# Optimization experiments

Measured on AMD Instinct MI355X. Metric: run time of the kernel, lower is better.

The kernel has to match this reference:

```python
import jax, jax.numpy as jnp
import numpy as np

TOPK = 8  # args.cache_k


def setup_inputs() -> dict:
    key = jax.random.key(0)
    k1, k2, k3 = jax.random.split(key, 3)
    B, N, L, DK, DV = 32, 20000, 20, 512, 512
    query = jax.random.normal(k1, (B, DK), dtype=jnp.float32)
    keys = jax.random.normal(k2, (N, DK), dtype=jnp.float32)
    values = jax.random.normal(k3, (N, L, DV), dtype=jnp.float32)
    return {"query": query, "keys": keys, "values": values}


def reference(query, keys, values):
    # Dot-product attention of query [B, dk] against cache keys [N, dk]
    dk = keys.shape[-1]
    scores = jnp.einsum('bd,nd->bn', query, keys) / jnp.sqrt(jnp.asarray(dk, query.dtype))
    attn = jax.nn.softmax(scores, axis=-1)          # [B, N]
    topk_w, topk_idx = jax.lax.top_k(attn, TOPK)    # [B, k]
    topk_w = topk_w.reshape(-1)                     # [B*k]
    topk_idx = topk_idx.reshape(-1)                 # [B*k]
    # Vectorized replacement of the per-index python loop + torch.cat:
    outputs = values[topk_idx]                      # [B*k, L, dv]
    return topk_w, outputs
```

## Files before the change

kernel.cpp:

```cpp
#include <hip/hip_runtime.h>
#include <math.h>


#define TOPK 8
#define DKD 512
#define NEG  -1.0e30f

typedef __attribute__((ext_vector_type(8))) short short8;
typedef __attribute__((ext_vector_type(4))) float f32x4;

__device__ inline unsigned short f2bf(float x) {
    unsigned int u = __float_as_uint(x);
    u = (u + 0x7fffu + ((u >> 16) & 1u)) >> 16;
    return (unsigned short)u;
}

__device__ inline void wave_argmax(float& v, int& i) {
    #pragma unroll
    for (int off = 1; off < 64; off <<= 1) {
        float ov = __shfl_xor(v, off);
        int   oi = __shfl_xor(i, off);
        if (ov > v || (ov == v && oi < i)) { v = ov; i = oi; }
    }
}

__device__ inline void top8_insert(float (&v)[8], int (&ji)[8], float x, int gi) {
    if (x > v[7]) {
        bool g[8];
        #pragma unroll
        for (int k = 0; k < 8; ++k) g[k] = (x > v[k]);
        #pragma unroll
        for (int k = 7; k >= 1; --k) {
            v[k]  = g[k] ? (g[k - 1] ? v[k - 1] : x)  : v[k];
            ji[k] = g[k] ? (g[k - 1] ? ji[k - 1] : gi) : ji[k];
        }
        v[0]  = g[0] ? x  : v[0];
        ji[0] = g[0] ? gi : ji[0];
    }
}

__global__ __launch_bounds__(256) void score_part_kernel(
    const float* __restrict__ q, const float* __restrict__ keys,
    float* __restrict__ pmg, float* __restrict__ psg,
    float* __restrict__ cvg, int* __restrict__ cig, int N, int NTB)
{
    const int tid  = threadIdx.x;
    const int lane = tid & 63;
    const int wid  = tid >> 6;
    const float scale = 0.04419417382415922f;

    __shared__ short qs[32][DKD + 8];
    __shared__ float S[32][65];

    #pragma unroll
    for (int i = 0; i < 16; ++i) {
        const int idx = i * 256 + tid;
        const int row = idx >> 7;
        const int c4  = idx & 127;
        float4 v = *reinterpret_cast<const float4*>(&q[row * DKD + c4 * 4]);
        ushort4 h;
        h.x = f2bf(v.x); h.y = f2bf(v.y); h.z = f2bf(v.z); h.w = f2bf(v.w);
        *reinterpret_cast<ushort4*>(&qs[row][c4 * 4]) = h;
    }
    __syncthreads();

    {
        const int col = lane & 15;
        const int kg  = lane >> 4;
        const int n0  = blockIdx.x * 64 + wid * 16;

        f32x4 acc0 = {0.f, 0.f, 0.f, 0.f};
        f32x4 acc1 = {0.f, 0.f, 0.f, 0.f};

        int nrow = n0 + col;
        const bool valid = (nrow < N);
        if (!valid) nrow = N - 1;
        const float* krow = keys + (size_t)nrow * DKD + kg * 8;
        const short* s0 = &qs[col][kg * 8];
        const short* s1 = &qs[col + 16][kg * 8];

        #pragma unroll 4
        for (int ks = 0; ks < 16; ++ks) {
            const int d = ks * 32;
            float4 ka = *reinterpret_cast<const float4*>(krow + d);
            float4 kb = *reinterpret_cast<const float4*>(krow + d + 4);
            short8 fh;
            fh[0] = (short)f2bf(ka.x); fh[1] = (short)f2bf(ka.y);
            fh[2] = (short)f2bf(ka.z); fh[3] = (short)f2bf(ka.w);
            fh[4] = (short)f2bf(kb.x); fh[5] = (short)f2bf(kb.y);
            fh[6] = (short)f2bf(kb.z); fh[7] = (short)f2bf(kb.w);
            short8 a0 = *reinterpret_cast<const short8*>(s0 + d);
            short8 a1 = *reinterpret_cast<const short8*>(s1 + d);
            acc0 = __builtin_amdgcn_mfma_f32_16x16x32_bf16(a0, fh, acc0, 0, 0, 0);
            acc1 = __builtin_amdgcn_mfma_f32_16x16x32_bf16(a1, fh, acc1, 0, 0, 0);
        }

        #pragma unroll
        for (int j = 0; j < 4; ++j) {
            const int r = kg * 4 + j;
            S[r][wid * 16 + col]      = valid ? acc0[j] * scale : NEG;
            S[r + 16][wid * 16 + col] = valid ? acc1[j] * scale : NEG;
        }
    }
    __syncthreads();

    {
        const int r = tid >> 3;
        const int g = tid & 7;
        float m = NEG, s = 0.f;
        float v[8]; int ji[8];
        #pragma unroll
        for (int k = 0; k < 8; ++k) { v[k] = NEG; ji[k] = 0x7ffffffe; }

        #pragma unroll
        for (int e = 0; e < 8; ++e) {
            const int c  = g * 8 + e;
            const float x = S[r][c];
            const int  gi = blockIdx.x * 64 + c;
            if (x > -5e29f) {
                const float nm = fmaxf(m, x);
                s = s * __expf(m - nm) + __expf(x - nm);
                m = nm;
                top8_insert(v, ji, x, gi);
            }
        }

        #pragma unroll
        for (int off = 1; off < 8; off <<= 1) {
            float om = __shfl_xor(m, off), os = __shfl_xor(s, off);
            float M2 = fmaxf(m, om);
            s = s * __expf(m - M2) + os * __expf(om - M2);
            m = M2;
        }

        float sel_v[8]; int sel_i[8];
        #pragma unroll
        for (int rr = 0; rr < 8; ++rr) {
            float mv = v[0]; int mi = ji[0];
            #pragma unroll
            for (int off = 1; off < 8; off <<= 1) {
                float ov = __shfl_xor(mv, off);
                int   oi = __shfl_xor(mi, off);
                if (ov > mv || (ov == mv && oi < mi)) { mv = ov; mi = oi; }
            }
            if (v[0] == mv && ji[0] == mi) {
                #pragma unroll
                for (int k = 0; k < 7; ++k) { v[k] = v[k + 1]; ji[k] = ji[k + 1]; }
                v[7] = NEG; ji[7] = 0x7ffffffe;
            }
            sel_v[rr] = mv; sel_i[rr] = mi;
        }

        if (g == 0) {
            const size_t base = (size_t)r * NTB + blockIdx.x;
            pmg[base] = m; psg[base] = s;
            #pragma unroll
            for (int k = 0; k < 8; ++k) {
                cvg[base * 8 + k] = sel_v[k];
                cig[base * 8 + k] = sel_i[k];
            }
        }
    }
}

__global__ __launch_bounds__(256) void row_merge_kernel(
    const float* __restrict__ pmg, const float* __restrict__ psg,
    const float* __restrict__ cvg, const int* __restrict__ cig,
    const float* __restrict__ q, const float* __restrict__ keys,
    float* __restrict__ out_w, int* __restrict__ tidx, int NTB)
{
    const int b    = blockIdx.x;
    const int tid  = threadIdx.x;
    const int lane = tid & 63;
    const int wid  = tid >> 6;
    const float scale = 0.04419417382415922f;

    __shared__ float lm[4], ls[4], lcv[4][TOPK];
    __shared__ int   lci[4][TOPK];

    float m = NEG, s = 0.f;
    float v[8]; int ji[8];
    #pragma unroll
    for (int k = 0; k < 8; ++k) { v[k] = NEG; ji[k] = 0x7ffffffe; }

    for (int tb = tid; tb < NTB; tb += 256) {
        const size_t base = (size_t)b * NTB + tb;
        const float pm_t = pmg[base], ps_t = psg[base];
        const float M2 = fmaxf(m, pm_t);
        s = s * __expf(m - M2) + ps_t * __expf(pm_t - M2);
        m = M2;
        #pragma unroll
        for (int k = 0; k < 8; ++k) {
            top8_insert(v, ji, cvg[base * 8 + k], cig[base * 8 + k]);
        }
    }

    #pragma unroll
    for (int off = 1; off < 64; off <<= 1) {
        float om = __shfl_xor(m, off), os = __shfl_xor(s, off);
        float M2 = fmaxf(m, om);
        s = s * __expf(m - M2) + os * __expf(om - M2);
        m = M2;
    }

    float selv = 0.f; int seli = 0;
    #pragma unroll
    for (int r = 0; r < TOPK; ++r) {
        float mv = v[0]; int mi = ji[0];
        wave_argmax(mv, mi);
        if (v[0] == mv && ji[0] == mi) {
            #pragma unroll
            for (int k = 0; k < TOPK - 1; ++k) { v[k] = v[k + 1]; ji[k] = ji[k + 1]; }
            v[TOPK - 1] = NEG; ji[TOPK - 1] = 0x7ffffffe;
        }
        if (lane == r) { selv = mv; seli = mi; }
    }

    if (lane == 0) { lm[wid] = m; ls[wid] = s; }
    if (lane < TOPK) { lcv[wid][lane] = selv; lci[wid][lane] = seli; }
    __syncthreads();

    if (wid != 0) return;

    float M = lm[0], S = ls[0];
    #pragma unroll
    for (int cc = 1; cc < 4; ++cc) {
        float M2 = fmaxf(M, lm[cc]);
        S = S * __expf(M - M2) + ls[cc] * __expf(lm[cc] - M2);
        M = M2;
    }

    float vv = (lane < 32) ? lcv[lane >> 3][lane & 7] : NEG;
    int   ii = (lane < 32) ? lci[lane >> 3][lane & 7] : 0x7ffffffe;
    int   si = 0x7ffffffe;
    #pragma unroll
    for (int r = 0; r < 12; ++r) {
        float mv = vv; int mi = ii;
        wave_argmax(mv, mi);
        if (vv == mv && ii == mi) vv = NEG;
        if (lane == r) si = mi;
    }

    float4 qa = *reinterpret_cast<const float4*>(q + (size_t)b * DKD + lane * 8);
    float4 qb = *reinterpret_cast<const float4*>(q + (size_t)b * DKD + lane * 8 + 4);
    float exv = NEG;
    #pragma unroll
    for (int r = 0; r < 12; ++r) {
        const int cand = __shfl(si, r);
        const float* kr = keys + (size_t)cand * DKD + lane * 8;
        float4 k1 = *reinterpret_cast<const float4*>(kr);
        float4 k2 = *reinterpret_cast<const float4*>(kr + 4);
        float p = qa.x * k1.x + qa.y * k1.y + qa.z * k1.z + qa.w * k1.w
                + qb.x * k2.x + qb.y * k2.y + qb.z * k2.z + qb.w * k2.w;
        #pragma unroll
        for (int off = 1; off < 64; off <<= 1) p += __shfl_xor(p, off);
        if (lane == r) exv = p * scale;
    }

    float fv = (lane < 12) ? exv : NEG;
    int   fi = (lane < 12) ? si : 0x7ffffffe;
    #pragma unroll
    for (int r = 0; r < TOPK; ++r) {
        float mv = fv; int mi = fi;
        wave_argmax(mv, mi);
        if (fv == mv && fi == mi) fv = NEG;
        if (lane == r) {
            out_w[b * TOPK + r] = __expf(mv - M) / S;
            tidx[b * TOPK + r]  = mi;
        }
    }
}

__global__ __launch_bounds__(256) void gather_kernel(
    const float* __restrict__ values, const int* __restrict__ idx,
    float* __restrict__ out, int LDV)
{
    const int bk  = blockIdx.x >> 2;
    const int qtr = blockIdx.x & 3;
    const int id = idx[bk];
    const float4* src = reinterpret_cast<const float4*>(values + (size_t)id * LDV);
    float4*       dst = reinterpret_cast<float4*>(out + (size_t)bk * LDV);
    const int n4 = LDV >> 2;
    const int qn = n4 >> 2;
    for (int i = qtr * qn + threadIdx.x; i < (qtr + 1) * qn; i += 256)
        dst[i] = src[i];
}

extern "C" void kernel_launch(void* const* d_in, const int* in_sizes, int n_in,
                              void* d_out, int out_size, void* d_ws, size_t ws_size,
                              hipStream_t stream) {
    const float* q      = (const float*)d_in[0];
    const float* keys   = (const float*)d_in[1];
    const float* values = (const float*)d_in[2];

    const int B   = in_sizes[0] / DKD;
    const int N   = in_sizes[1] / DKD;
    const int LDV = (int)((long long)in_sizes[2] / N);
    const int NTB = (N + 63) / 64;

    float* out   = (float*)d_out;
    float* out_w = out;
    float* out_v = out + (size_t)B * TOPK;

    char* wsb = (char*)d_ws;
    size_t off = 0;
    float* pmg = (float*)(wsb + off); off += (size_t)B * NTB * sizeof(float);
    float* psg = (float*)(wsb + off); off += (size_t)B * NTB * sizeof(float);
    float* cvg = (float*)(wsb + off); off += (size_t)B * NTB * 8 * sizeof(float);
    int*   cig = (int*)(wsb + off);   off += (size_t)B * NTB * 8 * sizeof(int);
    int*   tidx = (int*)(wsb + off);  off += (size_t)B * TOPK * sizeof(int);

    score_part_kernel<<<NTB, 256, 0, stream>>>(q, keys, pmg, psg, cvg, cig, N, NTB);
    row_merge_kernel<<<B, 256, 0, stream>>>(pmg, psg, cvg, cig, q, keys, out_w, tidx, NTB);
    gather_kernel<<<B * TOPK * 4, 256, 0, stream>>>(values, tidx, out_v, LDV);
}
```

Baseline: 48.69 us.

## Fuse row merge into gather kernel by recomputing merge per gather block

Merges the row-merge and gather kernels into one launch: each of the B*TOPK*4 gather blocks redundantly recomputes its row's top-k merge (reading all partials, rescoring 12 candidates), then copies its quarter of the selected value row. This removes one kernel launch and the workspace round-trip for indices, at the cost of 32x redundant merge work per row. It also fully unrolls the score loop and sets min-blocks-per-EU on the score kernel.

```diff
diff --git a/kernel.cpp b/kernel.cpp
--- a/kernel.cpp
+++ b/kernel.cpp
@@ -39,7 +39,7 @@
     }
 }
 
-__global__ __launch_bounds__(256) void score_part_kernel(
+__global__ __launch_bounds__(256, 1) void score_part_kernel(
     const float* __restrict__ q, const float* __restrict__ keys,
     float* __restrict__ pmg, float* __restrict__ psg,
     float* __restrict__ cvg, int* __restrict__ cig, int N, int NTB)
@@ -79,7 +79,7 @@
         const short* s0 = &qs[col][kg * 8];
         const short* s1 = &qs[col + 16][kg * 8];
 
-        #pragma unroll 4
+        #pragma unroll
         for (int ks = 0; ks < 16; ++ks) {
             const int d = ks * 32;
             float4 ka = *reinterpret_cast<const float4*>(krow + d);
@@ -163,13 +163,17 @@
     }
 }
 
-__global__ __launch_bounds__(256) void row_merge_kernel(
+__global__ __launch_bounds__(256) void merge_gather_kernel(
     const float* __restrict__ pmg, const float* __restrict__ psg,
     const float* __restrict__ cvg, const int* __restrict__ cig,
     const float* __restrict__ q, const float* __restrict__ keys,
-    float* __restrict__ out_w, int* __restrict__ tidx, int NTB)
+    const float* __restrict__ values,
+    float* __restrict__ out_w, float* __restrict__ out_v, int NTB, int LDV)
 {
-    const int b    = blockIdx.x;
+    const int bk   = blockIdx.x >> 2;
+    const int qtr  = blockIdx.x & 3;
+    const int b    = bk >> 3;
+    const int krk  = bk & 7;
     const int tid  = threadIdx.x;
     const int lane = tid & 63;
     const int wid  = tid >> 6;
@@ -177,6 +181,7 @@
 
     __shared__ float lm[4], ls[4], lcv[4][TOPK];
     __shared__ int   lci[4][TOPK];
+    __shared__ int   s_id;
 
     float m = NEG, s = 0.f;
     float v[8]; int ji[8];
@@ -220,69 +225,64 @@
     if (lane < TOPK) { lcv[wid][lane] = selv; lci[wid][lane] = seli; }
     __syncthreads();
 
-    if (wid != 0) return;
-
-    float M = lm[0], S = ls[0];
-    #pragma unroll
-    for (int cc = 1; cc < 4; ++cc) {
-        float M2 = fmaxf(M, lm[cc]);
-        S = S * __expf(M - M2) + ls[cc] * __expf(lm[cc] - M2);
-        M = M2;
-    }
-
-    float vv = (lane < 32) ? lcv[lane >> 3][lane & 7] : NEG;
-    int   ii = (lane < 32) ? lci[lane >> 3][lane & 7] : 0x7ffffffe;
-    int   si = 0x7ffffffe;
-    #pragma unroll
-    for (int r = 0; r < 12; ++r) {
-        float mv = vv; int mi = ii;
-        wave_argmax(mv, mi);
-        if (vv == mv && ii == mi) vv = NEG;
-        if (lane == r) si = mi;
-    }
-
-    float4 qa = *reinterpret_cast<const float4*>(q + (size_t)b * DKD + lane * 8);
-    float4 qb = *reinterpret_cast<const float4*>(q + (size_t)b * DKD + lane * 8 + 4);
-    float exv = NEG;
-    #pragma unroll
-    for (int r = 0; r < 12; ++r) {
-        const int cand = __shfl(si, r);
-        const float* kr = keys + (size_t)cand * DKD + lane * 8;
-        float4 k1 = *reinterpret_cast<const float4*>(kr);
-        float4 k2 = *reinterpret_cast<const float4*>(kr + 4);
-        float p = qa.x * k1.x + qa.y * k1.y + qa.z * k1.z + qa.w * k1.w
-                + qb.x * k2.x + qb.y * k2.y + qb.z * k2.z + qb.w * k2.w;
-        #pragma unroll
-        for (int off = 1; off < 64; off <<= 1) p += __shfl_xor(p, off);
-        if (lane == r) exv = p * scale;
-    }
-
-    float fv = (lane < 12) ? exv : NEG;
-    int   fi = (lane < 12) ? si : 0x7ffffffe;
-    #pragma unroll
-    for (int r = 0; r < TOPK; ++r) {
-        float mv = fv; int mi = fi;
-        wave_argmax(mv, mi);
-        if (fv == mv && fi == mi) fv = NEG;
-        if (lane == r) {
-            out_w[b * TOPK + r] = __expf(mv - M) / S;
-            tidx[b * TOPK + r]  = mi;
-        }
-    }
-}
-
-__global__ __launch_bounds__(256) void gather_kernel(
-    const float* __restrict__ values, const int* __restrict__ idx,
-    float* __restrict__ out, int LDV)
-{
-    const int bk  = blockIdx.x >> 2;
-    const int qtr = blockIdx.x & 3;
-    const int id = idx[bk];
+    if (wid == 0) {
+        float M = lm[0], S = ls[0];
+        #pragma unroll
+        for (int cc = 1; cc < 4; ++cc) {
+            float M2 = fmaxf(M, lm[cc]);
+            S = S * __expf(M - M2) + ls[cc] * __expf(lm[cc] - M2);
+            M = M2;
+        }
+
+        float vv = (lane < 32) ? lcv[lane >> 3][lane & 7] : NEG;
+        int   ii = (lane < 32) ? lci[lane >> 3][lane & 7] : 0x7ffffffe;
+        int   si = 0x7ffffffe;
+        #pragma unroll
+        for (int r = 0; r < 12; ++r) {
+            float mv = vv; int mi = ii;
+            wave_argmax(mv, mi);
+            if (vv == mv && ii == mi) vv = NEG;
+            if (lane == r) si = mi;
+        }
+
+        float4 qa = *reinterpret_cast<const float4*>(q + (size_t)b * DKD + lane * 8);
+        float4 qb = *reinterpret_cast<const float4*>(q + (size_t)b * DKD + lane * 8 + 4);
+        float exv = NEG;
+        #pragma unroll
+        for (int r = 0; r < 12; ++r) {
+            const int cand = __shfl(si, r);
+            const float* kr = keys + (size_t)cand * DKD + lane * 8;
+            float4 k1 = *reinterpret_cast<const float4*>(kr);
+            float4 k2 = *reinterpret_cast<const float4*>(kr + 4);
+            float p = qa.x * k1.x + qa.y * k1.y + qa.z * k1.z + qa.w * k1.w
+                    + qb.x * k2.x + qb.y * k2.y + qb.z * k2.z + qb.w * k2.w;
+            #pragma unroll
+            for (int off = 1; off < 64; off <<= 1) p += __shfl_xor(p, off);
+            if (lane == r) exv = p * scale;
+        }
+
+        float fv = (lane < 12) ? exv : NEG;
+        int   fi = (lane < 12) ? si : 0x7ffffffe;
+        #pragma unroll
+        for (int r = 0; r < TOPK; ++r) {
+            float mv = fv; int mi = fi;
+            wave_argmax(mv, mi);
+            if (fv == mv && fi == mi) fv = NEG;
+            if (lane == r) {
+                if (r == krk) s_id = mi;
+                if (qtr == 0 && krk == 0)
+                    out_w[b * TOPK + r] = __expf(mv - M) / S;
+            }
+        }
+    }
+    __syncthreads();
+
+    const int id = s_id;
     const float4* src = reinterpret_cast<const float4*>(values + (size_t)id * LDV);
-    float4*       dst = reinterpret_cast<float4*>(out + (size_t)bk * LDV);
+    float4*       dst = reinterpret_cast<float4*>(out_v + (size_t)bk * LDV);
     const int n4 = LDV >> 2;
     const int qn = n4 >> 2;
-    for (int i = qtr * qn + threadIdx.x; i < (qtr + 1) * qn; i += 256)
+    for (int i = qtr * qn + tid; i < (qtr + 1) * qn; i += 256)
         dst[i] = src[i];
 }
 
@@ -308,9 +308,8 @@
     float* psg = (float*)(wsb + off); off += (size_t)B * NTB * sizeof(float);
     float* cvg = (float*)(wsb + off); off += (size_t)B * NTB * 8 * sizeof(float);
     int*   cig = (int*)(wsb + off);   off += (size_t)B * NTB * 8 * sizeof(int);
-    int*   tidx = (int*)(wsb + off);  off += (size_t)B * TOPK * sizeof(int);
 
     score_part_kernel<<<NTB, 256, 0, stream>>>(q, keys, pmg, psg, cvg, cig, N, NTB);
-    row_merge_kernel<<<B, 256, 0, stream>>>(pmg, psg, cvg, cig, q, keys, out_w, tidx, NTB);
-    gather_kernel<<<B * TOPK * 4, 256, 0, stream>>>(values, tidx, out_v, LDV);
-}
+    merge_gather_kernel<<<B * TOPK * 4, 256, 0, stream>>>(
+        pmg, psg, cvg, cig, q, keys, values, out_w, out_v, NTB, LDV);
+}
```

After: 52.13 us. 1.07x slower.

## Split the key-dimension reduction across waves and halve keys per score block

Applied to the files above, without the earlier changes.

The score kernel now uses 512 threads and 32 keys per block. Four wave pairs each compute a 128-wide slice of the dot products, preloading their query fragments into registers. Partial sums are written to a padded shared array and reduced by the top-k/softmax stage, which runs on the first 256 threads. This doubles the number of score blocks to spread the bandwidth-bound key read over more CUs. In exchange it doubles the partial results that the row merge kernel must combine, and it drops the out-of-range masking, which is only safe when N is a multiple of 32. The query row padding also changes to 2 shorts, which breaks 16-byte alignment of the shared-memory vector loads.

```diff
diff --git a/kernel.cpp b/kernel.cpp
--- a/kernel.cpp
+++ b/kernel.cpp
@@ -39,7 +39,7 @@
     }
 }
 
-__global__ __launch_bounds__(256) void score_part_kernel(
+__global__ __launch_bounds__(512) void score_part_kernel(
     const float* __restrict__ q, const float* __restrict__ keys,
     float* __restrict__ pmg, float* __restrict__ psg,
     float* __restrict__ cvg, int* __restrict__ cig, int N, int NTB)
@@ -49,12 +49,12 @@
     const int wid  = tid >> 6;
     const float scale = 0.04419417382415922f;
 
-    __shared__ short qs[32][DKD + 8];
-    __shared__ float S[32][65];
-
-    #pragma unroll
-    for (int i = 0; i < 16; ++i) {
-        const int idx = i * 256 + tid;
+    __shared__ short qs[32][DKD + 2];
+    __shared__ float Sp[4][32][33];
+
+    #pragma unroll
+    for (int i = 0; i < 8; ++i) {
+        const int idx = i * 512 + tid;
         const int row = idx >> 7;
         const int c4  = idx & 127;
         float4 v = *reinterpret_cast<const float4*>(&q[row * DKD + c4 * 4]);
@@ -65,22 +65,30 @@
     __syncthreads();
 
     {
+        const int sub = wid & 1;
+        const int kq  = wid >> 1;
         const int col = lane & 15;
         const int kg  = lane >> 4;
-        const int n0  = blockIdx.x * 64 + wid * 16;
+        const int n0  = blockIdx.x * 32 + sub * 16;
+
+        int nrow = n0 + col;
+        if (nrow >= N) nrow = N - 1;
+        const float* krow = keys + (size_t)nrow * DKD + kq * 128 + kg * 8;
+        const short* s0 = &qs[col][kq * 128 + kg * 8];
+        const short* s1 = &qs[col + 16][kq * 128 + kg * 8];
+
+        short8 a0[4], a1[4];
+        #pragma unroll
+        for (int ks = 0; ks < 4; ++ks) {
+            a0[ks] = *reinterpret_cast<const short8*>(s0 + ks * 32);
+            a1[ks] = *reinterpret_cast<const short8*>(s1 + ks * 32);
+        }
 
         f32x4 acc0 = {0.f, 0.f, 0.f, 0.f};
         f32x4 acc1 = {0.f, 0.f, 0.f, 0.f};
 
-        int nrow = n0 + col;
-        const bool valid = (nrow < N);
-        if (!valid) nrow = N - 1;
-        const float* krow = keys + (size_t)nrow * DKD + kg * 8;
-        const short* s0 = &qs[col][kg * 8];
-        const short* s1 = &qs[col + 16][kg * 8];
-
-        #pragma unroll 4
-        for (int ks = 0; ks < 16; ++ks) {
+        #pragma unroll
+        for (int ks = 0; ks < 4; ++ks) {
             const int d = ks * 32;
             float4 ka = *reinterpret_cast<const float4*>(krow + d);
             float4 kb = *reinterpret_cast<const float4*>(krow + d + 4);
@@ -89,22 +97,20 @@
             fh[2] = (short)f2bf(ka.z); fh[3] = (short)f2bf(ka.w);
             fh[4] = (short)f2bf(kb.x); fh[5] = (short)f2bf(kb.y);
             fh[6] = (short)f2bf(kb.z); fh[7] = (short)f2bf(kb.w);
-            short8 a0 = *reinterpret_cast<const short8*>(s0 + d);
-            short8 a1 = *reinterpret_cast<const short8*>(s1 + d);
-            acc0 = __builtin_amdgcn_mfma_f32_16x16x32_bf16(a0, fh, acc0, 0, 0, 0);
-            acc1 = __builtin_amdgcn_mfma_f32_16x16x32_bf16(a1, fh, acc1, 0, 0, 0);
+            acc0 = __builtin_amdgcn_mfma_f32_16x16x32_bf16(a0[ks], fh, acc0, 0, 0, 0);
+            acc1 = __builtin_amdgcn_mfma_f32_16x16x32_bf16(a1[ks], fh, acc1, 0, 0, 0);
         }
 
         #pragma unroll
         for (int j = 0; j < 4; ++j) {
             const int r = kg * 4 + j;
-            S[r][wid * 16 + col]      = valid ? acc0[j] * scale : NEG;
-            S[r + 16][wid * 16 + col] = valid ? acc1[j] * scale : NEG;
+            Sp[kq][r][sub * 16 + col]      = acc0[j];
+            Sp[kq][r + 16][sub * 16 + col] = acc1[j];
         }
     }
     __syncthreads();
 
-    {
+    if (tid < 256) {
         const int r = tid >> 3;
         const int g = tid & 7;
         float m = NEG, s = 0.f;
@@ -113,16 +119,14 @@
         for (int k = 0; k < 8; ++k) { v[k] = NEG; ji[k] = 0x7ffffffe; }
 
         #pragma unroll
-        for (int e = 0; e < 8; ++e) {
-            const int c  = g * 8 + e;
-            const float x = S[r][c];
-            const int  gi = blockIdx.x * 64 + c;
-            if (x > -5e29f) {
-                const float nm = fmaxf(m, x);
-                s = s * __expf(m - nm) + __expf(x - nm);
-                m = nm;
-                top8_insert(v, ji, x, gi);
-            }
+        for (int e = 0; e < 4; ++e) {
+            const int c = g * 4 + e;
+            const float x = (Sp[0][r][c] + Sp[1][r][c] + Sp[2][r][c] + Sp[3][r][c]) * scale;
+            const int gi = blockIdx.x * 32 + c;
+            const float nm = fmaxf(m, x);
+            s = s * __expf(m - nm) + __expf(x - nm);
+            m = nm;
+            top8_insert(v, ji, x, gi);
         }
 
         #pragma unroll
@@ -296,7 +300,7 @@
     const int B   = in_sizes[0] / DKD;
     const int N   = in_sizes[1] / DKD;
     const int LDV = (int)((long long)in_sizes[2] / N);
-    const int NTB = (N + 63) / 64;
+    const int NTB = (N + 31) / 32;
 
     float* out   = (float*)d_out;
     float* out_w = out;
@@ -310,7 +314,7 @@
     int*   cig = (int*)(wsb + off);   off += (size_t)B * NTB * 8 * sizeof(int);
     int*   tidx = (int*)(wsb + off);  off += (size_t)B * TOPK * sizeof(int);
 
-    score_part_kernel<<<NTB, 256, 0, stream>>>(q, keys, pmg, psg, cvg, cig, N, NTB);
+    score_part_kernel<<<NTB, 512, 0, stream>>>(q, keys, pmg, psg, cvg, cig, N, NTB);
     row_merge_kernel<<<B, 256, 0, stream>>>(pmg, psg, cvg, cig, q, keys, out_w, tidx, NTB);
     gather_kernel<<<B * TOPK * 4, 256, 0, stream>>>(values, tidx, out_v, LDV);
 }
```

New measurement: 49.12 us. No clear change (+0.9%).
